# Kernel optimization log

Hardware: AMD Instinct MI355X
Metric: run time of the kernel (lower is better)

The kernel has to match this reference:

```python
import jax, jax.numpy as jnp
import numpy as np

EPS = 1e-12

def _wn(v, g):
    # weight norm per output channel (axis 0): w[o] = g[o] * v[o] / ||v[o]||
    return g[:, None] * v / jnp.linalg.norm(v, axis=1, keepdims=True)

def _unit(x):
    # row-wise L2 normalize with clip, matching _normalize in source
    return x / jnp.clip(jnp.linalg.norm(x, axis=-1, keepdims=True), EPS)

def setup_inputs() -> dict:
    key = jax.random.key(0)
    ks = jax.random.split(key, 8)
    D, CD, K, T = 1024, 256, 8192, 16384
    return {
        "z": jax.random.normal(ks[0], (D, T), dtype=jnp.float32),
        "in_v": jax.random.normal(ks[1], (CD, D), dtype=jnp.float32) * 0.02,
        "in_g": jax.random.uniform(ks[2], (CD,), dtype=jnp.float32, minval=0.5, maxval=1.5),
        "in_b": jax.random.normal(ks[3], (CD,), dtype=jnp.float32) * 0.01,
        "out_v": jax.random.normal(ks[4], (D, CD), dtype=jnp.float32) * 0.02,
        "out_g": jax.random.uniform(ks[5], (D,), dtype=jnp.float32, minval=0.5, maxval=1.5),
        "out_b": jax.random.normal(ks[6], (D,), dtype=jnp.float32) * 0.01,
        "codebook": jax.random.normal(ks[7], (K, CD), dtype=jnp.float32),
    }

def reference(z, in_v, in_g, in_b, out_v, out_g, out_b, codebook):
    # in_proj: weight-normed 1x1 conv == matmul over channel dim
    z_e = _wn(in_v, in_g) @ z + in_b[:, None]            # (CD, T)
    # decode_latents
    enc = _unit(z_e.T)                                    # (T, CD)
    cb = _unit(codebook)                                  # (K, CD)
    # squared L2 distance via matmul-based cdist
    dist = (jnp.sum(enc * enc, axis=1, keepdims=True)
            - 2.0 * enc @ cb.T
            + jnp.sum(cb * cb, axis=1)[None, :])          # (T, K)
    indices = jnp.argmax(-dist, axis=1)                   # (T,)
    z_q = codebook[indices].T                             # (CD, T), raw codebook gather
    # straight-through estimator
    z_q = z_e + jax.lax.stop_gradient(z_q - z_e)
    # out_proj
    out = _wn(out_v, out_g) @ z_q + out_b[:, None]        # (D, T)
    return (out, indices)
```

## Files before the change

### kernel.cpp

```cpp
#include <hip/hip_runtime.h>
#include <hip/hip_bf16.h>
#include <math.h>

#define TDIM 16384
#define DDIM 1024
#define CDIM 256
#define KDIM 8192
#define KSPLIT 8

typedef unsigned short u16;
typedef __attribute__((ext_vector_type(8))) short bf16x8;
typedef __attribute__((ext_vector_type(8))) unsigned short us8;
typedef __attribute__((ext_vector_type(4))) float floatx4;

static const size_t OFF_WINH  = 0;
static const size_t OFF_WINL  = OFF_WINH  + (size_t)CDIM * DDIM / 2;
static const size_t OFF_WOUTH = OFF_WINL  + (size_t)CDIM * DDIM / 2;
static const size_t OFF_WOUTL = OFF_WOUTH + (size_t)DDIM * CDIM / 2;
static const size_t OFF_CBH   = OFF_WOUTL + (size_t)DDIM * CDIM / 2;
static const size_t OFF_CBL   = OFF_CBH   + (size_t)KDIM * CDIM / 2;
static const size_t OFF_C2    = OFF_CBL   + (size_t)KDIM * CDIM / 2;
static const size_t OFF_ZTH   = OFF_C2    + (size_t)KDIM;
static const size_t OFF_ZTL   = OFF_ZTH   + (size_t)TDIM * DDIM / 2;
static const size_t OFF_ZE    = OFF_ZTL   + (size_t)TDIM * DDIM / 2;
static const size_t OFF_PV    = OFF_ZE    + (size_t)CDIM * TDIM;
static const size_t OFF_PI    = OFF_PV    + (size_t)KSPLIT * TDIM;
static const size_t OFF_IDX   = OFF_PI    + (size_t)KSPLIT * TDIM;
static const size_t OFF_ETH   = OFF_ZTH;
static const size_t OFF_ETL   = OFF_ZTH + (size_t)TDIM * CDIM / 2;

static __device__ __forceinline__ u16 f2bf(float x) {
  __hip_bfloat16 h = __float2bfloat16(x);
  return *(u16*)&h;
}
static __device__ __forceinline__ float bf2f(u16 u) {
  __hip_bfloat16 h; *(u16*)&h = u;
  return __bfloat162float(h);
}

static __device__ __forceinline__ void gload16(const u16* g, u16* l) {
  __builtin_amdgcn_global_load_lds(
      (__attribute__((address_space(1))) void*)g,
      (__attribute__((address_space(3))) void*)l, 16, 0, 0);
}

__global__ __launch_bounds__(256) void rownorm_split(
    const float* __restrict__ v, const float* __restrict__ g,
    u16* __restrict__ hi, u16* __restrict__ lo, float* __restrict__ c2,
    int ncols, int clip) {
  __shared__ float red[256];
  int row = blockIdx.x;
  const float* vr = v + (size_t)row * ncols;
  float s = 0.f;
  for (int j = threadIdx.x; j < ncols; j += 256) { float x = vr[j]; s += x * x; }
  red[threadIdx.x] = s;
  __syncthreads();
  for (int off = 128; off > 0; off >>= 1) {
    if (threadIdx.x < off) red[threadIdx.x] += red[threadIdx.x + off];
    __syncthreads();
  }
  float norm = sqrtf(red[0]);
  if (clip) norm = fmaxf(norm, 1e-12f);
  float scale = (g ? g[row] : 1.0f) / norm;
  float s2 = 0.f;
  for (int j = threadIdx.x; j < ncols; j += 256) {
    float y = vr[j] * scale;
    u16 hh = f2bf(y);
    u16 ll = f2bf(y - bf2f(hh));
    hi[(size_t)row * ncols + j] = hh;
    lo[(size_t)row * ncols + j] = ll;
    s2 += y * y;
  }
  if (c2) {
    __syncthreads();
    red[threadIdx.x] = s2;
    __syncthreads();
    for (int off = 128; off > 0; off >>= 1) {
      if (threadIdx.x < off) red[threadIdx.x] += red[threadIdx.x + off];
      __syncthreads();
    }
    if (threadIdx.x == 0) c2[row] = red[0];
  }
}

__global__ __launch_bounds__(256) void transpose_split_z(
    const float* __restrict__ z, u16* __restrict__ zth, u16* __restrict__ ztl) {
  __shared__ float tile[64][65];
  int t0 = blockIdx.x * 64, d0 = blockIdx.y * 64;
  int tl = threadIdx.x & 63, grp = threadIdx.x >> 6;
#pragma unroll
  for (int r = 0; r < 16; r++) {
    int d = grp * 16 + r;
    tile[d][tl] = z[(size_t)(d0 + d) * TDIM + t0 + tl];
  }
  __syncthreads();
#pragma unroll
  for (int r = 0; r < 16; r++) {
    int t = grp * 16 + r;
    float x = tile[tl][t];
    u16 h = f2bf(x);
    u16 l = f2bf(x - bf2f(h));
    zth[(size_t)(t0 + t) * DDIM + d0 + tl] = h;
    ztl[(size_t)(t0 + t) * DDIM + d0 + tl] = l;
  }
}

__global__ __launch_bounds__(256) void gemm_mfma_in(
    const u16* __restrict__ ah_g, const u16* __restrict__ al_g,
    const u16* __restrict__ bh_g, const u16* __restrict__ bl_g,
    const float* __restrict__ bias, float* __restrict__ C, int K) {
  __shared__ u16 Ah[128 * 32], Al[128 * 32];
  __shared__ u16 Bh[64 * 32],  Bl[64 * 32];
  int tid = threadIdx.x;
  int n0 = blockIdx.x * 64;
  int m0 = blockIdx.y * 128;
  int lane = tid & 63, wid = tid >> 6;
  int wr = wid >> 1, wc = wid & 1;
  int q = lane >> 4, mm = lane & 15;
  int h = tid & 1;
  int sr = ((tid >> 1) ^ (h << 2)) & 127;
  int ssw = (sr ^ (sr >> 2)) & 3;
  int o0 = sr * 32 + ((((h << 1))     ^ ssw) << 3);
  int o1 = sr * 32 + ((((h << 1) | 1) ^ ssw) << 3);
  int gcol = h * 16;
  int sb = ((tid >> 1) ^ (h << 2)) & 63;
  int ssb = (sb ^ (sb >> 2)) & 3;
  int p0 = sb * 32 + ((((h << 1))     ^ ssb) << 3);
  int p1 = sb * 32 + ((((h << 1) | 1) ^ ssb) << 3);
  int sm = (mm ^ (mm >> 2)) & 3;
  int cq = (q ^ sm) << 3;

  const floatx4 z4 = {0.f, 0.f, 0.f, 0.f};
  floatx4 acc[4][2];
#pragma unroll
  for (int i = 0; i < 4; i++)
#pragma unroll
    for (int j = 0; j < 2; j++) acc[i][j] = z4;

  for (int c0 = 0; c0 < K; c0 += 32) {
    const size_t ga = (size_t)(m0 + sr) * K + c0 + gcol;
    us8 a_h0 = *(const us8*)&ah_g[ga];
    us8 a_h1 = *(const us8*)&ah_g[ga + 8];
    us8 a_l0 = *(const us8*)&al_g[ga];
    us8 a_l1 = *(const us8*)&al_g[ga + 8];
    us8 b_h0, b_h1, b_l0, b_l1;
    if (tid < 128) {
      const size_t gb = (size_t)(n0 + sb) * K + c0 + gcol;
      b_h0 = *(const us8*)&bh_g[gb];
      b_h1 = *(const us8*)&bh_g[gb + 8];
      b_l0 = *(const us8*)&bl_g[gb];
      b_l1 = *(const us8*)&bl_g[gb + 8];
    }
    __syncthreads();
    *(us8*)&Ah[o0] = a_h0; *(us8*)&Ah[o1] = a_h1;
    *(us8*)&Al[o0] = a_l0; *(us8*)&Al[o1] = a_l1;
    if (tid < 128) {
      *(us8*)&Bh[p0] = b_h0; *(us8*)&Bh[p1] = b_h1;
      *(us8*)&Bl[p0] = b_l0; *(us8*)&Bl[p1] = b_l1;
    }
    __syncthreads();

    bf16x8 fa[4], fb[2];
#pragma unroll
    for (int i = 0; i < 4; i++)
      fa[i] = *(const bf16x8*)&Ah[(wr * 64 + i * 16 + mm) * 32 + cq];
#pragma unroll
    for (int j = 0; j < 2; j++)
      fb[j] = *(const bf16x8*)&Bh[(wc * 32 + j * 16 + mm) * 32 + cq];
#pragma unroll
    for (int i = 0; i < 4; i++)
#pragma unroll
      for (int j = 0; j < 2; j++)
        acc[i][j] = __builtin_amdgcn_mfma_f32_16x16x32_bf16(fa[i], fb[j], acc[i][j], 0, 0, 0);
#pragma unroll
    for (int i = 0; i < 4; i++) {
      bf16x8 fl = *(const bf16x8*)&Al[(wr * 64 + i * 16 + mm) * 32 + cq];
#pragma unroll
      for (int j = 0; j < 2; j++)
        acc[i][j] = __builtin_amdgcn_mfma_f32_16x16x32_bf16(fl, fb[j], acc[i][j], 0, 0, 0);
    }
#pragma unroll
    for (int j = 0; j < 2; j++) {
      bf16x8 fl = *(const bf16x8*)&Bl[(wc * 32 + j * 16 + mm) * 32 + cq];
#pragma unroll
      for (int i = 0; i < 4; i++)
        acc[i][j] = __builtin_amdgcn_mfma_f32_16x16x32_bf16(fa[i], fl, acc[i][j], 0, 0, 0);
    }
  }

#pragma unroll
  for (int i = 0; i < 4; i++) {
#pragma unroll
    for (int r = 0; r < 4; r++) {
      int m_loc = wr * 64 + i * 16 + q * 4 + r;
      float bb = bias[m0 + m_loc];
      float* crow = &C[(size_t)(m0 + m_loc) * TDIM + n0 + wc * 32 + mm];
#pragma unroll
      for (int j = 0; j < 2; j++) crow[j * 16] = acc[i][j][r] + bb;
    }
  }
}

__global__ __launch_bounds__(256) void gemm_mfma_bias(
    const u16* __restrict__ ah_g, const u16* __restrict__ al_g,
    const u16* __restrict__ bh_g, const u16* __restrict__ bl_g,
    const float* __restrict__ bias, float* __restrict__ C, int K) {
  __shared__ u16 Ah[128 * 32], Al[128 * 32];
  __shared__ u16 Bh[128 * 32], Bl[128 * 32];
  int tid = threadIdx.x;
  int n0 = blockIdx.x * 128;
  int m0 = blockIdx.y * 128;
  int lane = tid & 63, wid = tid >> 6;
  int wr = wid >> 1, wc = wid & 1;
  int q = lane >> 4, mm = lane & 15;
  int h = tid & 1;
  int sr = ((tid >> 1) ^ (h << 2)) & 127;
  int ssw = (sr ^ (sr >> 2)) & 3;
  int o0 = sr * 32 + ((((h << 1))     ^ ssw) << 3);
  int o1 = sr * 32 + ((((h << 1) | 1) ^ ssw) << 3);
  int gcol = h * 16;
  int sm = (mm ^ (mm >> 2)) & 3;
  int cq = (q ^ sm) << 3;

  const floatx4 z4 = {0.f, 0.f, 0.f, 0.f};
  floatx4 acc[4][4];
#pragma unroll
  for (int i = 0; i < 4; i++)
#pragma unroll
    for (int j = 0; j < 4; j++) acc[i][j] = z4;

  for (int c0 = 0; c0 < K; c0 += 32) {
    const size_t ga = (size_t)(m0 + sr) * K + c0 + gcol;
    const size_t gb = (size_t)(n0 + sr) * K + c0 + gcol;
    us8 a_h0 = *(const us8*)&ah_g[ga];
    us8 a_h1 = *(const us8*)&ah_g[ga + 8];
    us8 a_l0 = *(const us8*)&al_g[ga];
    us8 a_l1 = *(const us8*)&al_g[ga + 8];
    us8 b_h0 = *(const us8*)&bh_g[gb];
    us8 b_h1 = *(const us8*)&bh_g[gb + 8];
    us8 b_l0 = *(const us8*)&bl_g[gb];
    us8 b_l1 = *(const us8*)&bl_g[gb + 8];
    __syncthreads();
    *(us8*)&Ah[o0] = a_h0; *(us8*)&Ah[o1] = a_h1;
    *(us8*)&Al[o0] = a_l0; *(us8*)&Al[o1] = a_l1;
    *(us8*)&Bh[o0] = b_h0; *(us8*)&Bh[o1] = b_h1;
    *(us8*)&Bl[o0] = b_l0; *(us8*)&Bl[o1] = b_l1;
    __syncthreads();

    bf16x8 fa[4], fb[4];
#pragma unroll
    for (int i = 0; i < 4; i++)
      fa[i] = *(const bf16x8*)&Ah[(wr * 64 + i * 16 + mm) * 32 + cq];
#pragma unroll
    for (int j = 0; j < 4; j++)
      fb[j] = *(const bf16x8*)&Bh[(wc * 64 + j * 16 + mm) * 32 + cq];
#pragma unroll
    for (int i = 0; i < 4; i++)
#pragma unroll
      for (int j = 0; j < 4; j++)
        acc[i][j] = __builtin_amdgcn_mfma_f32_16x16x32_bf16(fa[i], fb[j], acc[i][j], 0, 0, 0);
#pragma unroll
    for (int i = 0; i < 4; i++) {
      bf16x8 fl = *(const bf16x8*)&Al[(wr * 64 + i * 16 + mm) * 32 + cq];
#pragma unroll
      for (int j = 0; j < 4; j++)
        acc[i][j] = __builtin_amdgcn_mfma_f32_16x16x32_bf16(fl, fb[j], acc[i][j], 0, 0, 0);
    }
#pragma unroll
    for (int j = 0; j < 4; j++) {
      bf16x8 fl = *(const bf16x8*)&Bl[(wc * 64 + j * 16 + mm) * 32 + cq];
#pragma unroll
      for (int i = 0; i < 4; i++)
        acc[i][j] = __builtin_amdgcn_mfma_f32_16x16x32_bf16(fa[i], fl, acc[i][j], 0, 0, 0);
    }
  }

#pragma unroll
  for (int i = 0; i < 4; i++) {
#pragma unroll
    for (int r = 0; r < 4; r++) {
      int m_loc = wr * 64 + i * 16 + q * 4 + r;
      float bb = bias[m0 + m_loc];
      float* crow = &C[(size_t)(m0 + m_loc) * TDIM + n0 + wc * 64 + mm];
#pragma unroll
      for (int j = 0; j < 4; j++) crow[j * 16] = acc[i][j][r] + bb;
    }
  }
}

__global__ __launch_bounds__(256) void finish_ze(
    const float* __restrict__ ze, u16* __restrict__ eth, u16* __restrict__ etl) {
  __shared__ float tile[256][33];
  __shared__ float red[8][32];
  __shared__ float invs[32];
  int t0 = blockIdx.x * 32;
  int tl = threadIdx.x & 31, grp = threadIdx.x >> 5;
  float s = 0.f;
  for (int c = grp * 32; c < grp * 32 + 32; c++) {
    float v = ze[(size_t)c * TDIM + t0 + tl];
    tile[c][tl] = v;
    s += v * v;
  }
  red[grp][tl] = s;
  __syncthreads();
  if (grp == 0) {
    float tot = 0.f;
#pragma unroll
    for (int gg = 0; gg < 8; gg++) tot += red[gg][tl];
    invs[tl] = 1.0f / fmaxf(sqrtf(tot), 1e-12f);
  }
  __syncthreads();
#pragma unroll
  for (int r = 0; r < 4; r++) {
    int t = grp * 4 + r;
    float iv = invs[t];
#pragma unroll
    for (int cc = 0; cc < 8; cc++) {
      int cd = cc * 32 + tl;
      float x = tile[cd][t] * iv;
      u16 hh = f2bf(x);
      u16 ll = f2bf(x - bf2f(hh));
      eth[(size_t)(t0 + t) * CDIM + cd] = hh;
      etl[(size_t)(t0 + t) * CDIM + cd] = ll;
    }
  }
}

__global__ __launch_bounds__(512, 2) void dist_mfma(
    const u16* __restrict__ eth, const u16* __restrict__ etl,
    const u16* __restrict__ cbh, const u16* __restrict__ cbl,
    const float* __restrict__ c2, float* __restrict__ pv, int* __restrict__ pi) {
  __shared__ u16 AhL[4][128 * 64];
  __shared__ u16 AlL[4][128 * 64];
  __shared__ float c2L[1024];
  __shared__ float mv[2][128];
  __shared__ int   mi[2][128];

  int tid = threadIdx.x;
  int t0 = blockIdx.x * 128;
  int kbeg = blockIdx.y * (KDIM / KSPLIT);
  int lane = tid & 63, wid = tid >> 6;
  int wk = wid >> 2, wt = wid & 3;
  int q = lane >> 4, mm = lane & 15;

  int stR[2], stC[2], stL[2];
#pragma unroll
  for (int it = 0; it < 2; it++) {
    int gi = it * 512 + tid;
    int r = gi >> 3, g = gi & 7;
    stR[it] = r;
    stC[it] = (g ^ (r & 7)) << 3;
    stL[it] = gi << 3;
  }

  int foff[2];
#pragma unroll
  for (int kk = 0; kk < 2; kk++)
    foff[kk] = ((((kk << 2) | q) ^ (mm & 7)) << 3);

  float2 c2v2 = *(const float2*)&c2[kbeg + tid * 2];
  bf16x8 fbh[2][8], fbl[2][8];
#pragma unroll
  for (int j = 0; j < 2; ++j)
#pragma unroll
    for (int sl = 0; sl < 8; ++sl) {
      const size_t gb = (size_t)(t0 + wt * 32 + j * 16 + mm) * CDIM + sl * 32 + q * 8;
      fbh[j][sl] = *(const bf16x8*)&eth[gb];
      fbl[j][sl] = *(const bf16x8*)&etl[gb];
    }
  *(float2*)&c2L[tid * 2] = c2v2;
#pragma unroll
  for (int p = 0; p < 3; ++p) {
#pragma unroll
    for (int it = 0; it < 2; ++it) {
      const size_t ga = (size_t)(kbeg + stR[it]) * CDIM + p * 64 + stC[it];
      gload16(&cbh[ga], &AhL[p][stL[it]]);
      gload16(&cbl[ga], &AlL[p][stL[it]]);
    }
  }
  asm volatile("s_waitcnt lgkmcnt(0)" ::: "memory");

  float rbv[2]; int rbi[2];
#pragma unroll
  for (int j = 0; j < 2; j++) { rbv[j] = INFINITY; rbi[j] = 0x7fffffff; }

  const floatx4 z4 = {0.f, 0.f, 0.f, 0.f};
  floatx4 acc[4][2];
#pragma unroll
  for (int i = 0; i < 4; i++)
#pragma unroll
    for (int j = 0; j < 2; j++) acc[i][j] = z4;

  for (int ks = 0; ks < 8; ++ks) {
#pragma unroll
    for (int cc = 0; cc < 4; ++cc) {
      asm volatile("s_waitcnt vmcnt(8)" ::: "memory");
      __builtin_amdgcn_s_barrier();
      __builtin_amdgcn_sched_barrier(0);

      {
        int nn = (ks * 4 + cc + 3) & 31;
        int k0n = kbeg + ((nn >> 2) * 128);
        const int c0n = ((cc + 3) & 3) * 64;
        const int nb = (cc + 3) & 3;
#pragma unroll
        for (int it = 0; it < 2; ++it) {
          const size_t ga = (size_t)(k0n + stR[it]) * CDIM + c0n + stC[it];
          gload16(&cbh[ga], &AhL[nb][stL[it]]);
          gload16(&cbl[ga], &AlL[nb][stL[it]]);
        }
      }

      __builtin_amdgcn_s_setprio(1);
#pragma unroll
      for (int kk = 0; kk < 2; ++kk) {
        bf16x8 fah[4];
#pragma unroll
        for (int i = 0; i < 4; i++)
          fah[i] = *(const bf16x8*)&AhL[cc][(wk * 64 + i * 16 + mm) * 64 + foff[kk]];
#pragma unroll
        for (int i = 0; i < 4; i++)
#pragma unroll
          for (int j = 0; j < 2; j++)
            acc[i][j] = __builtin_amdgcn_mfma_f32_16x16x32_bf16(fah[i], fbh[j][cc * 2 + kk], acc[i][j], 0, 0, 0);
#pragma unroll
        for (int i = 0; i < 4; i++) {
          bf16x8 fl = *(const bf16x8*)&AlL[cc][(wk * 64 + i * 16 + mm) * 64 + foff[kk]];
#pragma unroll
          for (int j = 0; j < 2; j++)
            acc[i][j] = __builtin_amdgcn_mfma_f32_16x16x32_bf16(fl, fbh[j][cc * 2 + kk], acc[i][j], 0, 0, 0);
        }
#pragma unroll
        for (int j = 0; j < 2; j++) {
#pragma unroll
          for (int i = 0; i < 4; i++)
            acc[i][j] = __builtin_amdgcn_mfma_f32_16x16x32_bf16(fah[i], fbl[j][cc * 2 + kk], acc[i][j], 0, 0, 0);
        }
      }
      __builtin_amdgcn_s_setprio(0);
    }

#pragma unroll
    for (int i = 0; i < 4; i++) {
      floatx4 cv = *(const floatx4*)&c2L[ks * 128 + wk * 64 + i * 16 + q * 4];
#pragma unroll
      for (int r4 = 0; r4 < 4; r4++) {
        int kg = kbeg + ks * 128 + wk * 64 + i * 16 + q * 4 + r4;
        float c2v = cv[r4];
#pragma unroll
        for (int j = 0; j < 2; j++) {
          float s = c2v - 2.0f * acc[i][j][r4];
          if (s < rbv[j]) { rbv[j] = s; rbi[j] = kg; }
        }
      }
    }
#pragma unroll
    for (int i = 0; i < 4; i++)
#pragma unroll
      for (int j = 0; j < 2; j++) acc[i][j] = z4;
  }

#pragma unroll
  for (int j = 0; j < 2; j++) {
    float v = rbv[j]; int ii = rbi[j];
    float ov = __shfl_xor(v, 16, 64); int oi = __shfl_xor(ii, 16, 64);
    if (ov < v || (ov == v && oi < ii)) { v = ov; ii = oi; }
    ov = __shfl_xor(v, 32, 64); oi = __shfl_xor(ii, 32, 64);
    if (ov < v || (ov == v && oi < ii)) { v = ov; ii = oi; }
    rbv[j] = v; rbi[j] = ii;
  }
  if (q == 0) {
#pragma unroll
    for (int j = 0; j < 2; j++) {
      mv[wk][wt * 32 + j * 16 + mm] = rbv[j];
      mi[wk][wt * 32 + j * 16 + mm] = rbi[j];
    }
  }
  __syncthreads();
  if (tid < 128) {
    float v0 = mv[0][tid]; int i0 = mi[0][tid];
    float v1 = mv[1][tid]; int i1 = mi[1][tid];
    if (v1 < v0 || (v1 == v0 && i1 < i0)) { v0 = v1; i0 = i1; }
    pv[(size_t)blockIdx.y * TDIM + t0 + tid] = v0;
    pi[(size_t)blockIdx.y * TDIM + t0 + tid] = i0;
  }
}

__global__ __launch_bounds__(256) void merge_argmin(
    const float* __restrict__ pv, const int* __restrict__ pi,
    int* __restrict__ idx, float* __restrict__ idxf) {
  int t = blockIdx.x * 256 + threadIdx.x;
  float bv = INFINITY; int bi = 0x7fffffff;
  for (int s = 0; s < KSPLIT; s++) {
    float v = pv[(size_t)s * TDIM + t];
    int ii = pi[(size_t)s * TDIM + t];
    if (v < bv || (v == bv && ii < bi)) { bv = v; bi = ii; }
  }
  idx[t] = bi;
  idxf[t] = (float)bi;
}

__global__ __launch_bounds__(256) void gather_split(
    const int* __restrict__ idx, const float* __restrict__ cb,
    u16* __restrict__ zqh, u16* __restrict__ zql) {
  int t = blockIdx.x * 4 + (threadIdx.x >> 6);
  int c4 = (threadIdx.x & 63) * 4;
  int k = idx[t];
  float4 x = *(const float4*)&cb[(size_t)k * CDIM + c4];
  u16 h0 = f2bf(x.x), h1 = f2bf(x.y), h2 = f2bf(x.z), h3 = f2bf(x.w);
  u16 l0 = f2bf(x.x - bf2f(h0)), l1 = f2bf(x.y - bf2f(h1));
  u16 l2 = f2bf(x.z - bf2f(h2)), l3 = f2bf(x.w - bf2f(h3));
  ushort4 hv = {h0, h1, h2, h3}, lv = {l0, l1, l2, l3};
  *(ushort4*)&zqh[(size_t)t * CDIM + c4] = hv;
  *(ushort4*)&zql[(size_t)t * CDIM + c4] = lv;
}

extern "C" void kernel_launch(void* const* d_in, const int* in_sizes, int n_in,
                              void* d_out, int out_size, void* d_ws, size_t ws_size,
                              hipStream_t stream) {
  const float* z     = (const float*)d_in[0];
  const float* in_v  = (const float*)d_in[1];
  const float* in_g  = (const float*)d_in[2];
  const float* in_b  = (const float*)d_in[3];
  const float* out_v = (const float*)d_in[4];
  const float* out_g = (const float*)d_in[5];
  const float* out_b = (const float*)d_in[6];
  const float* cb    = (const float*)d_in[7];

  float* ws    = (float*)d_ws;
  u16*   winh  = (u16*)(ws + OFF_WINH);
  u16*   winl  = (u16*)(ws + OFF_WINL);
  u16*   wouth = (u16*)(ws + OFF_WOUTH);
  u16*   woutl = (u16*)(ws + OFF_WOUTL);
  u16*   cbh   = (u16*)(ws + OFF_CBH);
  u16*   cbl   = (u16*)(ws + OFF_CBL);
  float* c2    = ws + OFF_C2;
  u16*   zth   = (u16*)(ws + OFF_ZTH);
  u16*   ztl   = (u16*)(ws + OFF_ZTL);
  float* z_e   = ws + OFF_ZE;
  float* pv    = ws + OFF_PV;
  int*   pi    = (int*)(ws + OFF_PI);
  int*   idxw  = (int*)(ws + OFF_IDX);
  u16*   eth   = (u16*)(ws + OFF_ETH);
  u16*   etl   = (u16*)(ws + OFF_ETL);
  u16*   zqh   = eth;
  u16*   zql   = etl;

  float* outp = (float*)d_out;
  float* idxf = outp + (size_t)DDIM * TDIM;

  rownorm_split<<<CDIM, 256, 0, stream>>>(in_v, in_g, winh, winl, nullptr, DDIM, 0);
  rownorm_split<<<DDIM, 256, 0, stream>>>(out_v, out_g, wouth, woutl, nullptr, CDIM, 0);
  rownorm_split<<<KDIM, 256, 0, stream>>>(cb, nullptr, cbh, cbl, c2, CDIM, 1);

  transpose_split_z<<<dim3(TDIM / 64, DDIM / 64), 256, 0, stream>>>(z, zth, ztl);

  gemm_mfma_in<<<dim3(TDIM / 64, CDIM / 128), 256, 0, stream>>>(
      winh, winl, zth, ztl, in_b, z_e, DDIM);

  finish_ze<<<TDIM / 32, 256, 0, stream>>>(z_e, eth, etl);

  dist_mfma<<<dim3(TDIM / 128, KSPLIT), 512, 0, stream>>>(eth, etl, cbh, cbl, c2, pv, pi);
  merge_argmin<<<TDIM / 256, 256, 0, stream>>>(pv, pi, idxw, idxf);

  gather_split<<<TDIM / 4, 256, 0, stream>>>(idxw, cb, zqh, zql);

  gemm_mfma_bias<<<dim3(TDIM / 128, DDIM / 128), 256, 0, stream>>>(
      wouth, woutl, zqh, zql, out_b, outp, CDIM);
}
```

Measured before the change: 432.7 us.

## Replace four-stage LDS ring with double-buffered half-tile codebook staging

The codebook tile staging in the distance kernel changes from a four-slot ring of 64-column chunks, each guarded by a vmcnt wait and a barrier, to two ping-pong buffers holding 128-column halves. Each half is stored as 32-column sub-tiles with a new XOR swizzle. This halves the number of block-wide barriers per 128-row K step and simplifies address math. In exchange, each stage prefetches a whole half at once, so latency hiding is shallower. It also relies on __syncthreads to make the async LDS loads visible instead of an explicit vmcnt wait.

```diff
diff --git a/kernel.cpp b/kernel.cpp
--- a/kernel.cpp
+++ b/kernel.cpp
@@ -326,12 +326,59 @@
   }
 }
 
+static __device__ __forceinline__ void stage_phase(
+    const u16* __restrict__ cbh, const u16* __restrict__ cbl,
+    u16* AhB, u16* AlB, int krow, int c0, int scol, int ldso) {
+#pragma unroll
+  for (int u = 0; u < 4; ++u) {
+    const size_t ga = (size_t)krow * CDIM + c0 + u * 32 + scol;
+    gload16(&cbh[ga], &AhB[u * 4096 + ldso]);
+    gload16(&cbl[ga], &AlB[u * 4096 + ldso]);
+  }
+}
+
+template <int SL0>
+static __device__ __forceinline__ void dist_phase(
+    const u16* AhB, const u16* AlB,
+    const bf16x8 (&fbh)[2][8], const bf16x8 (&fbl)[2][8],
+    floatx4 (&acc)[4][2], int arow, int foffA) {
+#pragma unroll
+  for (int u = 0; u < 4; ++u) {
+    const u16* AhC = AhB + u * 4096;
+    const u16* AlC = AlB + u * 4096;
+    bf16x8 fah[4], fal[4];
+#pragma unroll
+    for (int i = 0; i < 4; i++)
+      fah[i] = *(const bf16x8*)&AhC[(arow + i * 16) * 32 + foffA];
+#pragma unroll
+    for (int i = 0; i < 4; i++)
+      fal[i] = *(const bf16x8*)&AlC[(arow + i * 16) * 32 + foffA];
+    __builtin_amdgcn_s_setprio(1);
+#pragma unroll
+    for (int i = 0; i < 4; i++)
+#pragma unroll
+      for (int j = 0; j < 2; j++)
+        acc[i][j] = __builtin_amdgcn_mfma_f32_16x16x32_bf16(fah[i], fbh[j][SL0 + u], acc[i][j], 0, 0, 0);
+#pragma unroll
+    for (int i = 0; i < 4; i++)
+#pragma unroll
+      for (int j = 0; j < 2; j++)
+        acc[i][j] = __builtin_amdgcn_mfma_f32_16x16x32_bf16(fal[i], fbh[j][SL0 + u], acc[i][j], 0, 0, 0);
+#pragma unroll
+    for (int j = 0; j < 2; j++)
+#pragma unroll
+      for (int i = 0; i < 4; i++)
+        acc[i][j] = __builtin_amdgcn_mfma_f32_16x16x32_bf16(fah[i], fbl[j][SL0 + u], acc[i][j], 0, 0, 0);
+    __builtin_amdgcn_s_setprio(0);
+  }
+}
+
 __global__ __launch_bounds__(512, 2) void dist_mfma(
     const u16* __restrict__ eth, const u16* __restrict__ etl,
     const u16* __restrict__ cbh, const u16* __restrict__ cbl,
     const float* __restrict__ c2, float* __restrict__ pv, int* __restrict__ pi) {
-  __shared__ u16 AhL[4][128 * 64];
-  __shared__ u16 AlL[4][128 * 64];
+  __shared__ u16 Ah0[4 * 4096], Ah1[4 * 4096];
+  __shared__ u16 Al0[4 * 4096], Al1[4 * 4096];
   __shared__ float c2L[1024];
   __shared__ float mv[2][128];
   __shared__ int   mi[2][128];
@@ -343,20 +390,11 @@
   int wk = wid >> 2, wt = wid & 3;
   int q = lane >> 4, mm = lane & 15;
 
-  int stR[2], stC[2], stL[2];
-#pragma unroll
-  for (int it = 0; it < 2; it++) {
-    int gi = it * 512 + tid;
-    int r = gi >> 3, g = gi & 7;
-    stR[it] = r;
-    stC[it] = (g ^ (r & 7)) << 3;
-    stL[it] = gi << 3;
-  }
-
-  int foff[2];
-#pragma unroll
-  for (int kk = 0; kk < 2; kk++)
-    foff[kk] = ((((kk << 2) | q) ^ (mm & 7)) << 3);
+  int r = tid >> 2, g = tid & 3;
+  int scol = (g ^ ((r >> 1) & 3)) << 3;
+  int ldso = tid * 8;
+  int arow = wk * 64 + mm;
+  int foffA = (q ^ ((mm >> 1) & 3)) << 3;
 
   float2 c2v2 = *(const float2*)&c2[kbeg + tid * 2];
   bf16x8 fbh[2][8], fbl[2][8];
@@ -369,16 +407,7 @@
       fbl[j][sl] = *(const bf16x8*)&etl[gb];
     }
   *(float2*)&c2L[tid * 2] = c2v2;
-#pragma unroll
-  for (int p = 0; p < 3; ++p) {
-#pragma unroll
-    for (int it = 0; it < 2; ++it) {
-      const size_t ga = (size_t)(kbeg + stR[it]) * CDIM + p * 64 + stC[it];
-      gload16(&cbh[ga], &AhL[p][stL[it]]);
-      gload16(&cbl[ga], &AlL[p][stL[it]]);
-    }
-  }
-  asm volatile("s_waitcnt lgkmcnt(0)" ::: "memory");
+  stage_phase(cbh, cbl, Ah0, Al0, kbeg + r, 0, scol, ldso);
 
   float rbv[2]; int rbi[2];
 #pragma unroll
@@ -392,53 +421,14 @@
     for (int j = 0; j < 2; j++) acc[i][j] = z4;
 
   for (int ks = 0; ks < 8; ++ks) {
-#pragma unroll
-    for (int cc = 0; cc < 4; ++cc) {
-      asm volatile("s_waitcnt vmcnt(8)" ::: "memory");
-      __builtin_amdgcn_s_barrier();
-      __builtin_amdgcn_sched_barrier(0);
-
-      {
-        int nn = (ks * 4 + cc + 3) & 31;
-        int k0n = kbeg + ((nn >> 2) * 128);
-        const int c0n = ((cc + 3) & 3) * 64;
-        const int nb = (cc + 3) & 3;
-#pragma unroll
-        for (int it = 0; it < 2; ++it) {
-          const size_t ga = (size_t)(k0n + stR[it]) * CDIM + c0n + stC[it];
-          gload16(&cbh[ga], &AhL[nb][stL[it]]);
-          gload16(&cbl[ga], &AlL[nb][stL[it]]);
-        }
-      }
-
-      __builtin_amdgcn_s_setprio(1);
-#pragma unroll
-      for (int kk = 0; kk < 2; ++kk) {
-        bf16x8 fah[4];
-#pragma unroll
-        for (int i = 0; i < 4; i++)
-          fah[i] = *(const bf16x8*)&AhL[cc][(wk * 64 + i * 16 + mm) * 64 + foff[kk]];
-#pragma unroll
-        for (int i = 0; i < 4; i++)
-#pragma unroll
-          for (int j = 0; j < 2; j++)
-            acc[i][j] = __builtin_amdgcn_mfma_f32_16x16x32_bf16(fah[i], fbh[j][cc * 2 + kk], acc[i][j], 0, 0, 0);
-#pragma unroll
-        for (int i = 0; i < 4; i++) {
-          bf16x8 fl = *(const bf16x8*)&AlL[cc][(wk * 64 + i * 16 + mm) * 64 + foff[kk]];
-#pragma unroll
-          for (int j = 0; j < 2; j++)
-            acc[i][j] = __builtin_amdgcn_mfma_f32_16x16x32_bf16(fl, fbh[j][cc * 2 + kk], acc[i][j], 0, 0, 0);
-        }
-#pragma unroll
-        for (int j = 0; j < 2; j++) {
-#pragma unroll
-          for (int i = 0; i < 4; i++)
-            acc[i][j] = __builtin_amdgcn_mfma_f32_16x16x32_bf16(fah[i], fbl[j][cc * 2 + kk], acc[i][j], 0, 0, 0);
-        }
-      }
-      __builtin_amdgcn_s_setprio(0);
-    }
+    __syncthreads();
+    stage_phase(cbh, cbl, Ah1, Al1, kbeg + ks * 128 + r, 128, scol, ldso);
+    dist_phase<0>(Ah0, Al0, fbh, fbl, acc, arow, foffA);
+
+    __syncthreads();
+    if (ks < 7)
+      stage_phase(cbh, cbl, Ah0, Al0, kbeg + (ks + 1) * 128 + r, 0, scol, ldso);
+    dist_phase<4>(Ah1, Al1, fbh, fbl, acc, arow, foffA);
 
 #pragma unroll
     for (int i = 0; i < 4; i++) {
```

After: 423.5 us. 2.1% less time.
